# Optimization experiments

Hardware: AMD Instinct MI355X
Metric: run time of the kernel (lower is better)

Reference implementation:

```python
import jax, jax.numpy as jnp
import numpy as np

N_NODES = 100000
N_EDGES = 1600000
D_FEAT = 512
HIDDEN = 64
N_CLASS = 16
DROP_P = 0.5


def setup_inputs() -> dict:
    key = jax.random.key(0)
    ks = jax.random.split(key, 6)
    x = jax.random.normal(ks[0], (N_NODES, D_FEAT), dtype=jnp.float32)
    edge_index = jax.random.randint(ks[1], (2, N_EDGES), 0, N_NODES, dtype=jnp.int32)
    e_w = jax.random.uniform(ks[2], (N_EDGES,), dtype=jnp.float32)
    # Glorot-ish init for the two GCN layer weights, zero bias (PyG default)
    W1 = jax.random.normal(ks[3], (D_FEAT, HIDDEN), dtype=jnp.float32) / np.sqrt(D_FEAT)
    b1 = jnp.zeros((HIDDEN,), dtype=jnp.float32)
    W2 = jax.random.normal(ks[4], (HIDDEN, N_CLASS), dtype=jnp.float32) / np.sqrt(HIDDEN)
    b2 = jnp.zeros((N_CLASS,), dtype=jnp.float32)
    return {"x": x, "edge_index": edge_index, "e_w": e_w,
            "W1": W1, "b1": b1, "W2": W2, "b2": b2}


def _gcn_conv(x, src, dst, w, W, b, num_nodes):
    """PyG GCNConv: linear transform, then symmetric-normalized scatter-add."""
    h = x @ W                                   # [N, out]
    deg = jax.ops.segment_sum(w, dst, num_segments=num_nodes)   # weighted in-degree
    dis = jnp.where(deg > 0, jax.lax.rsqrt(jnp.maximum(deg, 1e-12)), 0.0)
    norm = dis[src] * w * dis[dst]              # [E_total]
    msg = h[src] * norm[:, None]                # gather + scale  [E_total, out]
    out = jax.ops.segment_sum(msg, dst, num_segments=num_nodes)  # scatter-add
    return out + b


def reference(x, edge_index, e_w, W1, b1, W2, b2):
    n = x.shape[0]
    # add self-loops with weight 1 (GCNConv default)
    loops = jnp.arange(n, dtype=edge_index.dtype)
    src = jnp.concatenate([edge_index[0], loops])
    dst = jnp.concatenate([edge_index[1], loops])
    w = jnp.concatenate([e_w, jnp.ones((n,), dtype=e_w.dtype)])

    h = _gcn_conv(x, src, dst, w, W1, b1, n)
    h = jax.nn.relu(h)
    # F.dropout default p=0.5, training=True: deterministic fixed mask here
    keep = jax.random.bernoulli(jax.random.key(42), 1.0 - DROP_P, h.shape)
    h = jnp.where(keep, h / (1.0 - DROP_P), 0.0)

    x_out = _gcn_conv(h, src, dst, w, W2, b2, n)
    return jax.nn.log_softmax(x_out, axis=1), x_out
```

## Files before the change

### kernel.cpp

```cpp
#include <hip/hip_runtime.h>
#include <stdint.h>

#define N_NODES 100000
#define N_EDGES 1600000
#define D_FEAT  512
#define HIDDEN  64
#define N_CLASS 16
#define CAP     64
#define NBKT    196
#define BCAP    10240
#define EPB     4096
#define NWG1    ((N_EDGES + EPB - 1) / EPB)
#define GEMM1_BLKS ((N_NODES + 127) / 128)

typedef __bf16 bf16_t;
typedef bf16_t bf16x8 __attribute__((ext_vector_type(8)));
typedef float  f32x4  __attribute__((ext_vector_type(4)));

__device__ __forceinline__ unsigned rotl32(unsigned x, int d) {
    return (x << d) | (x >> (32 - d));
}
__device__ __forceinline__ void tf_round(unsigned& x0, unsigned& x1, int r) {
    x0 += x1; x1 = rotl32(x1, r); x1 ^= x0;
}
__device__ __forceinline__ uint2 threefry_0_42(unsigned c0, unsigned c1) {
    const unsigned ks0 = 0u, ks1 = 42u, ks2 = 0x1BD11BDAu ^ 0u ^ 42u;
    unsigned x0 = c0 + ks0, x1 = c1 + ks1;
    tf_round(x0,x1,13); tf_round(x0,x1,15); tf_round(x0,x1,26); tf_round(x0,x1,6);
    x0 += ks1; x1 += ks2 + 1u;
    tf_round(x0,x1,17); tf_round(x0,x1,29); tf_round(x0,x1,16); tf_round(x0,x1,24);
    x0 += ks2; x1 += ks0 + 2u;
    tf_round(x0,x1,13); tf_round(x0,x1,15); tf_round(x0,x1,26); tf_round(x0,x1,6);
    x0 += ks0; x1 += ks1 + 3u;
    tf_round(x0,x1,17); tf_round(x0,x1,29); tf_round(x0,x1,16); tf_round(x0,x1,24);
    x0 += ks1; x1 += ks2 + 4u;
    tf_round(x0,x1,13); tf_round(x0,x1,15); tf_round(x0,x1,26); tf_round(x0,x1,6);
    x0 += ks2; x1 += ks0 + 5u;
    return make_uint2(x0, x1);
}

__launch_bounds__(256)
__global__ void k_prep_bin(const float* __restrict__ W1, bf16_t* __restrict__ Wfg,
                           const int* __restrict__ src, const int* __restrict__ dst,
                           const float* __restrict__ w,
                           int* __restrict__ bucket_cursor, int2* __restrict__ bkt) {
    __shared__ int hist[NBKT];
    __shared__ int binbase[NBKT];
    int tid = threadIdx.x;
    int bid = blockIdx.x;
    if (bid < 128) {
        int e = bid * 256 + tid;
        int k = e >> 6, col = e & 63;
        int kstep = k >> 5, gg = (k >> 3) & 3, e8 = k & 7;
        int cf = col >> 4, lane = (col & 15) | (gg << 4);
        Wfg[(((kstep << 2) + cf) << 9) + (lane << 3) + e8] = (bf16_t)W1[e];
        return;
    }
    int b0 = bid - 128;
    int c4 = b0 * (EPB / 4);
    for (int t = tid; t < NBKT; t += 256) hist[t] = 0;
    __syncthreads();
    int rk[16]; int dd[16];
    #pragma unroll
    for (int i = 0; i < EPB / 1024; ++i) {
        int e4 = c4 + tid + 256 * i;
        if (e4 * 4 < N_EDGES) {
            int4 d = ((const int4*)dst)[e4];
            dd[4*i+0] = d.x; dd[4*i+1] = d.y; dd[4*i+2] = d.z; dd[4*i+3] = d.w;
            rk[4*i+0] = atomicAdd(&hist[d.x >> 9], 1);
            rk[4*i+1] = atomicAdd(&hist[d.y >> 9], 1);
            rk[4*i+2] = atomicAdd(&hist[d.z >> 9], 1);
            rk[4*i+3] = atomicAdd(&hist[d.w >> 9], 1);
        }
    }
    __syncthreads();
    for (int t = tid; t < NBKT; t += 256)
        binbase[t] = hist[t] ? atomicAdd(&bucket_cursor[t], hist[t]) : 0;
    __syncthreads();
    #pragma unroll
    for (int i = 0; i < EPB / 1024; ++i) {
        int e4 = c4 + tid + 256 * i;
        if (e4 * 4 < N_EDGES) {
            int4 s  = ((const int4*)src)[e4];
            int4 wv = ((const int4*)w)[e4];
            int ss[4] = {s.x, s.y, s.z, s.w};
            int ww[4] = {wv.x, wv.y, wv.z, wv.w};
            #pragma unroll
            for (int q = 0; q < 4; ++q) {
                int d = dd[4*i+q];
                int b = d >> 9;
                int pos = binbase[b] + rk[4*i+q];
                if (pos < BCAP)
                    bkt[(size_t)b * BCAP + pos] =
                        make_int2(ss[q] | ((d & 511) << 17), ww[q]);
            }
        }
    }
}

__launch_bounds__(256)
__global__ void k_build_gemm1(const int* __restrict__ bucket_cursor,
                              const int2* __restrict__ bkt,
                              int2* __restrict__ slots, int* __restrict__ cursor,
                              float* __restrict__ dis,
                              const float* __restrict__ x,
                              const bf16_t* __restrict__ Wfg,
                              bf16_t* __restrict__ h1) {
    __shared__ __align__(16) char smem[32768];
    int tid = threadIdx.x;
    int bid = blockIdx.x;
    if (bid < NBKT) {
        int* cur  = (int*)smem;
        float* dg = (float*)(smem + 2048);
        int b = bid;
        cur[tid] = 0; cur[tid + 256] = 0;
        dg[tid] = 0.f; dg[tid + 256] = 0.f;
        __syncthreads();
        int cnt = bucket_cursor[b]; if (cnt > BCAP) cnt = BCAP;
        for (int e = tid; e < cnt; e += 256) {
            int2 p = bkt[(size_t)b * BCAP + e];
            int dl = ((unsigned)p.x) >> 17;
            int s  = p.x & 0x1FFFF;
            int rank = atomicAdd(&cur[dl], 1);
            if (rank < CAP)
                slots[((((size_t)b << 9) | dl) << 6) + rank] = make_int2(s, p.y);
            atomicAdd(&dg[dl], __int_as_float(p.y));
        }
        __syncthreads();
        #pragma unroll
        for (int t = 0; t < 2; ++t) {
            int loc = tid + 256 * t;
            int node = (b << 9) + loc;
            if (node < N_NODES) {
                cursor[node] = cur[loc];
                dis[node] = rsqrtf(dg[loc] + 1.0f);
            }
        }
        return;
    }
    bf16_t* Wf = (bf16_t*)smem;
    int gb = bid - NBKT;
    int w = tid >> 6, l = tid & 63;
    int r = l & 15, g = l >> 4;
    int wrow = gb * 128 + w * 32;
    f32x4 acc[2][4] = {};
    const float* xp0 = x + (size_t)(wrow + r) * D_FEAT + 8 * g;
    const float* xp1 = x + (size_t)(wrow + 16 + r) * D_FEAT + 8 * g;
    bool ok0 = (wrow + r) < N_NODES;
    bool ok1 = (wrow + 16 + r) < N_NODES;

    #pragma unroll
    for (int h = 0; h < 2; ++h) {
        if (h) __syncthreads();
        {
            const int4* sW = (const int4*)(Wfg + h * 16384);
            int4* dW = (int4*)Wf;
            #pragma unroll
            for (int t = 0; t < 8; ++t) dW[tid + 256 * t] = sW[tid + 256 * t];
        }
        __syncthreads();
        #pragma unroll
        for (int t2 = 0; t2 < 8; ++t2) {
            int t = h * 8 + t2;
            float4 p0 = make_float4(0.f,0.f,0.f,0.f), q0 = p0, p1 = p0, q1 = p0;
            if (ok0) {
                p0 = *(const float4*)(xp0 + t * 32);
                q0 = *(const float4*)(xp0 + t * 32 + 4);
            }
            if (ok1) {
                p1 = *(const float4*)(xp1 + t * 32);
                q1 = *(const float4*)(xp1 + t * 32 + 4);
            }
            bf16x8 a0, a1;
            a0[0]=(bf16_t)p0.x; a0[1]=(bf16_t)p0.y; a0[2]=(bf16_t)p0.z; a0[3]=(bf16_t)p0.w;
            a0[4]=(bf16_t)q0.x; a0[5]=(bf16_t)q0.y; a0[6]=(bf16_t)q0.z; a0[7]=(bf16_t)q0.w;
            a1[0]=(bf16_t)p1.x; a1[1]=(bf16_t)p1.y; a1[2]=(bf16_t)p1.z; a1[3]=(bf16_t)p1.w;
            a1[4]=(bf16_t)q1.x; a1[5]=(bf16_t)q1.y; a1[6]=(bf16_t)q1.z; a1[7]=(bf16_t)q1.w;
            #pragma unroll
            for (int cf = 0; cf < 4; ++cf) {
                bf16x8 b = *(const bf16x8*)&Wf[(((t2 << 2) + cf) << 9) + (l << 3)];
                acc[0][cf] = __builtin_amdgcn_mfma_f32_16x16x32_bf16(a0, b, acc[0][cf], 0, 0, 0);
                acc[1][cf] = __builtin_amdgcn_mfma_f32_16x16x32_bf16(a1, b, acc[1][cf], 0, 0, 0);
            }
        }
    }
    #pragma unroll
    for (int rf = 0; rf < 2; ++rf)
        #pragma unroll
        for (int cf = 0; cf < 4; ++cf)
            #pragma unroll
            for (int q = 0; q < 4; ++q) {
                int row = wrow + rf * 16 + 4 * g + q;
                int col = cf * 16 + r;
                if (row < N_NODES) h1[(size_t)row * HIDDEN + col] = (bf16_t)acc[rf][cf][q];
            }
}

__launch_bounds__(256)
__global__ void k_agg1(const bf16_t* __restrict__ h1, const int2* __restrict__ slots,
                       const int* __restrict__ cursor, const float* __restrict__ dis,
                       const float* __restrict__ b1, const float* __restrict__ W2,
                       bf16_t* __restrict__ g) {
    __shared__ float W2s[HIDDEN * 17];
    __shared__ float h2s[4][HIDDEN];
    int tid = threadIdx.x;
    #pragma unroll
    for (int t = 0; t < 4; ++t) {
        int e = tid + 256 * t;
        W2s[(e >> 4) * 17 + (e & 15)] = W2[e];
    }
    int i = (blockIdx.x * blockDim.x + tid) >> 6;
    int l = tid & 63;
    int w = tid >> 6;
    int h = l >> 5, s32 = l & 31;
    if (i < N_NODES) {
        float di = dis[i];
        int cnt = cursor[i]; cnt = cnt > CAP ? CAP : cnt;
        const int2* sl = &slots[(size_t)i << 6];
        float a0 = 0.f, a1 = 0.f;
        if (h == 0) {
            unsigned v = *(const unsigned*)&h1[(size_t)i * HIDDEN + 2 * s32];
            float n = di * di;
            a0 = n * __uint_as_float(v << 16);
            a1 = n * __uint_as_float(v & 0xffff0000u);
        }
        #pragma unroll 2
        for (int p = h; p < cnt; p += 2) {
            int2 e0 = sl[p];
            float n = dis[e0.x] * __int_as_float(e0.y) * di;
            unsigned v = *(const unsigned*)&h1[(size_t)e0.x * HIDDEN + 2 * s32];
            a0 += n * __uint_as_float(v << 16);
            a1 += n * __uint_as_float(v & 0xffff0000u);
        }
        a0 += __shfl_xor(a0, 32);
        a1 += __shfl_xor(a1, 32);
        int f = 2 * s32 + h;
        float av = h ? a1 : a0;
        av += b1[f];
        av = fmaxf(av, 0.f);
        unsigned idx = (unsigned)i * HIDDEN + f;
        uint2 rr = threefry_0_42(0u, idx);
        h2s[w][f] = ((rr.x ^ rr.y) & 0x80000000u) ? 0.f : av * 2.f;
    } else {
        h2s[w][2 * s32 + h] = 0.f;
    }
    __syncthreads();
    int j = tid & 15, q = (tid >> 4) & 3;
    int node = blockIdx.x * 4 + w;
    float p = 0.f;
    #pragma unroll
    for (int ff = 0; ff < 16; ++ff) {
        int fr = q * 16 + ff;
        p += h2s[w][fr] * W2s[fr * 17 + j];
    }
    p += __shfl_xor(p, 16, 64);
    p += __shfl_xor(p, 32, 64);
    if (q == 0 && node < N_NODES) g[(size_t)node * N_CLASS + j] = (bf16_t)p;
}

__launch_bounds__(256)
__global__ void k_out(const bf16_t* __restrict__ g, const int2* __restrict__ slots,
                      const int* __restrict__ cursor, const float* __restrict__ dis,
                      const float* __restrict__ b2, float* __restrict__ out) {
    int i = (blockIdx.x * blockDim.x + threadIdx.x) >> 4;
    int j = threadIdx.x & 15;
    if (i >= N_NODES) return;
    float di = dis[i];
    float acc = di * di * (float)g[(size_t)i * N_CLASS + j];
    int cnt = cursor[i]; cnt = cnt > CAP ? CAP : cnt;
    const int2* sl = &slots[(size_t)i << 6];
    int p = 0;
    for (; p + 2 <= cnt; p += 2) {
        int2 e0 = sl[p], e1 = sl[p+1];
        float n0 = dis[e0.x] * __int_as_float(e0.y) * di;
        float n1 = dis[e1.x] * __int_as_float(e1.y) * di;
        acc += n0 * (float)g[(size_t)e0.x * N_CLASS + j]
             + n1 * (float)g[(size_t)e1.x * N_CLASS + j];
    }
    for (; p < cnt; ++p) {
        int2 e0 = sl[p];
        acc += dis[e0.x] * __int_as_float(e0.y) * di * (float)g[(size_t)e0.x * N_CLASS + j];
    }
    acc += b2[j];
    float xo = acc;
    float m = acc;
    #pragma unroll
    for (int d = 1; d < 16; d <<= 1) m = fmaxf(m, __shfl_xor(m, d, 16));
    float ex = expf(acc - m);
    float s = ex;
    #pragma unroll
    for (int d = 1; d < 16; d <<= 1) s += __shfl_xor(s, d, 16);
    float ls = (acc - m) - logf(s);
    out[(size_t)i * N_CLASS + j] = ls;
    out[(size_t)N_NODES * N_CLASS + (size_t)i * N_CLASS + j] = xo;
}

extern "C" void kernel_launch(void* const* d_in, const int* in_sizes, int n_in,
                              void* d_out, int out_size, void* d_ws, size_t ws_size,
                              hipStream_t stream) {
    const float* x  = (const float*)d_in[0];
    const int*   ei = (const int*)d_in[1];
    const float* ew = (const float*)d_in[2];
    const float* W1 = (const float*)d_in[3];
    const float* b1 = (const float*)d_in[4];
    const float* W2 = (const float*)d_in[5];
    const float* b2 = (const float*)d_in[6];
    float* out = (float*)d_out;
    const int* src = ei;
    const int* dst = ei + N_EDGES;

    size_t off = 0;
    char* wsb = (char*)d_ws;
    auto alloc = [&](size_t n) -> char* {
        char* p = wsb + off;
        off = (off + n + 255) & ~(size_t)255;
        return p;
    };
    int*    cursor = (int*)   alloc((size_t)N_NODES * 4);
    float*  dis    = (float*) alloc((size_t)N_NODES * 4);
    int*    bcur   = (int*)   alloc(NBKT * 4);
    bf16_t* Wfg    = (bf16_t*)alloc(32768 * 2);
    int2*   slots  = (int2*)  alloc((size_t)N_NODES * CAP * 8);
    bf16_t* h1     = (bf16_t*)alloc((size_t)N_NODES * HIDDEN * 2);
    int2*   bkt    = (int2*)  alloc((size_t)NBKT * BCAP * 8);
    bf16_t* g      = (bf16_t*)alloc((size_t)N_NODES * N_CLASS * 2);

    hipMemsetAsync(bcur, 0, NBKT * 4, stream);

    k_prep_bin   <<<128 + NWG1, 256, 0, stream>>>(W1, Wfg, src, dst, ew, bcur, bkt);
    k_build_gemm1<<<NBKT + GEMM1_BLKS, 256, 0, stream>>>(bcur, bkt, slots, cursor, dis,
                                                         x, Wfg, h1);
    k_agg1<<<(N_NODES + 3) / 4, 256, 0, stream>>>(h1, slots, cursor, dis, b1, W2, g);
    k_out <<<(N_NODES * 16 + 255) / 256, 256, 0, stream>>>(g, slots, cursor, dis, b2, out);
}
```

Measured before the change: 204.0 us.

## Fold source-side degree normalization into GEMM output and split build from GEMM

Moves the dis[src] factor of the symmetric normalization into the producer side: the first GEMM scales each h1 row by dis[row], and k_agg1 scales its output g by dis[i]. The aggregation loops then multiply only by the raw edge weight, which removes a random gather of dis[src] per edge in both aggregation kernels. The destination factor is applied once per node after the sum. To make dis available to the GEMM, the fused build+GEMM launch is split into two kernels, giving up the overlap between bucket building and the GEMM and adding one launch, in exchange for the cheaper aggregation.

```diff
diff --git a/kernel.cpp b/kernel.cpp
--- a/kernel.cpp
+++ b/kernel.cpp
@@ -99,50 +99,45 @@
 }
 
 __launch_bounds__(256)
-__global__ void k_build_gemm1(const int* __restrict__ bucket_cursor,
-                              const int2* __restrict__ bkt,
-                              int2* __restrict__ slots, int* __restrict__ cursor,
-                              float* __restrict__ dis,
-                              const float* __restrict__ x,
-                              const bf16_t* __restrict__ Wfg,
-                              bf16_t* __restrict__ h1) {
-    __shared__ __align__(16) char smem[32768];
+__global__ void k_build(const int* __restrict__ bucket_cursor, const int2* __restrict__ bkt,
+                        int2* __restrict__ slots, int* __restrict__ cursor,
+                        float* __restrict__ dis) {
+    __shared__ int   cur[512];
+    __shared__ float dg[512];
+    int b = blockIdx.x, tid = threadIdx.x;
+    cur[tid] = 0; cur[tid + 256] = 0;
+    dg[tid] = 0.f; dg[tid + 256] = 0.f;
+    __syncthreads();
+    int cnt = bucket_cursor[b]; if (cnt > BCAP) cnt = BCAP;
+    for (int e = tid; e < cnt; e += 256) {
+        int2 p = bkt[(size_t)b * BCAP + e];
+        int dl = ((unsigned)p.x) >> 17;
+        int s  = p.x & 0x1FFFF;
+        int rank = atomicAdd(&cur[dl], 1);
+        if (rank < CAP)
+            slots[((((size_t)b << 9) | dl) << 6) + rank] = make_int2(s, p.y);
+        atomicAdd(&dg[dl], __int_as_float(p.y));
+    }
+    __syncthreads();
+    #pragma unroll
+    for (int t = 0; t < 2; ++t) {
+        int loc = tid + 256 * t;
+        int node = (b << 9) + loc;
+        if (node < N_NODES) {
+            cursor[node] = cur[loc];
+            dis[node] = rsqrtf(dg[loc] + 1.0f);
+        }
+    }
+}
+
+__launch_bounds__(256)
+__global__ void k_gemm1(const float* __restrict__ x, const bf16_t* __restrict__ Wfg,
+                        const float* __restrict__ dis, bf16_t* __restrict__ h1) {
+    __shared__ bf16_t Wf[16384];
     int tid = threadIdx.x;
-    int bid = blockIdx.x;
-    if (bid < NBKT) {
-        int* cur  = (int*)smem;
-        float* dg = (float*)(smem + 2048);
-        int b = bid;
-        cur[tid] = 0; cur[tid + 256] = 0;
-        dg[tid] = 0.f; dg[tid + 256] = 0.f;
-        __syncthreads();
-        int cnt = bucket_cursor[b]; if (cnt > BCAP) cnt = BCAP;
-        for (int e = tid; e < cnt; e += 256) {
-            int2 p = bkt[(size_t)b * BCAP + e];
-            int dl = ((unsigned)p.x) >> 17;
-            int s  = p.x & 0x1FFFF;
-            int rank = atomicAdd(&cur[dl], 1);
-            if (rank < CAP)
-                slots[((((size_t)b << 9) | dl) << 6) + rank] = make_int2(s, p.y);
-            atomicAdd(&dg[dl], __int_as_float(p.y));
-        }
-        __syncthreads();
-        #pragma unroll
-        for (int t = 0; t < 2; ++t) {
-            int loc = tid + 256 * t;
-            int node = (b << 9) + loc;
-            if (node < N_NODES) {
-                cursor[node] = cur[loc];
-                dis[node] = rsqrtf(dg[loc] + 1.0f);
-            }
-        }
-        return;
-    }
-    bf16_t* Wf = (bf16_t*)smem;
-    int gb = bid - NBKT;
     int w = tid >> 6, l = tid & 63;
     int r = l & 15, g = l >> 4;
-    int wrow = gb * 128 + w * 32;
+    int wrow = blockIdx.x * 128 + w * 32;
     f32x4 acc[2][4] = {};
     const float* xp0 = x + (size_t)(wrow + r) * D_FEAT + 8 * g;
     const float* xp1 = x + (size_t)(wrow + 16 + r) * D_FEAT + 8 * g;
@@ -187,13 +182,15 @@
     #pragma unroll
     for (int rf = 0; rf < 2; ++rf)
         #pragma unroll
-        for (int cf = 0; cf < 4; ++cf)
-            #pragma unroll
-            for (int q = 0; q < 4; ++q) {
-                int row = wrow + rf * 16 + 4 * g + q;
-                int col = cf * 16 + r;
-                if (row < N_NODES) h1[(size_t)row * HIDDEN + col] = (bf16_t)acc[rf][cf][q];
-            }
+        for (int q = 0; q < 4; ++q) {
+            int row = wrow + rf * 16 + 4 * g + q;
+            if (row < N_NODES) {
+                float dv = dis[row];
+                #pragma unroll
+                for (int cf = 0; cf < 4; ++cf)
+                    h1[(size_t)row * HIDDEN + cf * 16 + r] = (bf16_t)(dv * acc[rf][cf][q]);
+            }
+        }
 }
 
 __launch_bounds__(256)
@@ -213,21 +210,20 @@
     int l = tid & 63;
     int w = tid >> 6;
     int h = l >> 5, s32 = l & 31;
+    float di = (i < N_NODES) ? dis[i] : 0.f;
     if (i < N_NODES) {
-        float di = dis[i];
         int cnt = cursor[i]; cnt = cnt > CAP ? CAP : cnt;
         const int2* sl = &slots[(size_t)i << 6];
         float a0 = 0.f, a1 = 0.f;
         if (h == 0) {
             unsigned v = *(const unsigned*)&h1[(size_t)i * HIDDEN + 2 * s32];
-            float n = di * di;
-            a0 = n * __uint_as_float(v << 16);
-            a1 = n * __uint_as_float(v & 0xffff0000u);
+            a0 = __uint_as_float(v << 16);
+            a1 = __uint_as_float(v & 0xffff0000u);
         }
         #pragma unroll 2
         for (int p = h; p < cnt; p += 2) {
             int2 e0 = sl[p];
-            float n = dis[e0.x] * __int_as_float(e0.y) * di;
+            float n = __int_as_float(e0.y);
             unsigned v = *(const unsigned*)&h1[(size_t)e0.x * HIDDEN + 2 * s32];
             a0 += n * __uint_as_float(v << 16);
             a1 += n * __uint_as_float(v & 0xffff0000u);
@@ -235,8 +231,7 @@
         a0 += __shfl_xor(a0, 32);
         a1 += __shfl_xor(a1, 32);
         int f = 2 * s32 + h;
-        float av = h ? a1 : a0;
-        av += b1[f];
+        float av = di * (h ? a1 : a0) + b1[f];
         av = fmaxf(av, 0.f);
         unsigned idx = (unsigned)i * HIDDEN + f;
         uint2 rr = threefry_0_42(0u, idx);
@@ -255,7 +250,7 @@
     }
     p += __shfl_xor(p, 16, 64);
     p += __shfl_xor(p, 32, 64);
-    if (q == 0 && node < N_NODES) g[(size_t)node * N_CLASS + j] = (bf16_t)p;
+    if (q == 0 && node < N_NODES) g[(size_t)node * N_CLASS + j] = (bf16_t)(di * p);
 }
 
 __launch_bounds__(256)
@@ -266,22 +261,22 @@
     int j = threadIdx.x & 15;
     if (i >= N_NODES) return;
     float di = dis[i];
-    float acc = di * di * (float)g[(size_t)i * N_CLASS + j];
+    float acc = (float)g[(size_t)i * N_CLASS + j];
     int cnt = cursor[i]; cnt = cnt > CAP ? CAP : cnt;
     const int2* sl = &slots[(size_t)i << 6];
     int p = 0;
     for (; p + 2 <= cnt; p += 2) {
         int2 e0 = sl[p], e1 = sl[p+1];
-        float n0 = dis[e0.x] * __int_as_float(e0.y) * di;
-        float n1 = dis[e1.x] * __int_as_float(e1.y) * di;
+        float n0 = __int_as_float(e0.y);
+        float n1 = __int_as_float(e1.y);
         acc += n0 * (float)g[(size_t)e0.x * N_CLASS + j]
              + n1 * (float)g[(size_t)e1.x * N_CLASS + j];
     }
     for (; p < cnt; ++p) {
         int2 e0 = sl[p];
-        acc += dis[e0.x] * __int_as_float(e0.y) * di * (float)g[(size_t)e0.x * N_CLASS + j];
-    }
-    acc += b2[j];
+        acc += __int_as_float(e0.y) * (float)g[(size_t)e0.x * N_CLASS + j];
+    }
+    acc = di * acc + b2[j];
     float xo = acc;
     float m = acc;
     #pragma unroll
@@ -327,9 +322,9 @@
 
     hipMemsetAsync(bcur, 0, NBKT * 4, stream);
 
-    k_prep_bin   <<<128 + NWG1, 256, 0, stream>>>(W1, Wfg, src, dst, ew, bcur, bkt);
-    k_build_gemm1<<<NBKT + GEMM1_BLKS, 256, 0, stream>>>(bcur, bkt, slots, cursor, dis,
-                                                         x, Wfg, h1);
-    k_agg1<<<(N_NODES + 3) / 4, 256, 0, stream>>>(h1, slots, cursor, dis, b1, W2, g);
-    k_out <<<(N_NODES * 16 + 255) / 256, 256, 0, stream>>>(g, slots, cursor, dis, b2, out);
-}
+    k_prep_bin<<<128 + NWG1, 256, 0, stream>>>(W1, Wfg, src, dst, ew, bcur, bkt);
+    k_build   <<<NBKT, 256, 0, stream>>>(bcur, bkt, slots, cursor, dis);
+    k_gemm1   <<<GEMM1_BLKS, 256, 0, stream>>>(x, Wfg, dis, h1);
+    k_agg1    <<<(N_NODES + 3) / 4, 256, 0, stream>>>(h1, slots, cursor, dis, b1, W2, g);
+    k_out     <<<(N_NODES * 16 + 255) / 256, 256, 0, stream>>>(g, slots, cursor, dis, b2, out);
+}
```

After: 200.9 us. About the same (-1.5%).
